# Kernel optimization log

Measured on AMD Instinct MI355X. Metric: run time of the kernel, lower is better.

## Reference

```python
import jax, jax.numpy as jnp
import numpy as np

CHUNK = 128  # single steady-state chunk tier (T divisible by 128)
DECAY_MIN = 0.005


def setup_inputs() -> dict:
    key = jax.random.key(0)
    k0, k1, k2, k3, k4 = jax.random.split(key, 5)
    B, H, T, K = 4, 16, 2048, 64
    r = jax.random.normal(k0, (B, H, T, K), jnp.float32) * 0.5
    k = jax.random.normal(k1, (B, H, T, K), jnp.float32) * 0.5
    v = jax.random.normal(k2, (B, H, T, K), jnp.float32)
    # log-space decay (negative); mild magnitude keeps exp() of cumulative
    # in-chunk decays within fp32 range (torch original upcasts to fp64)
    w = -(jax.random.uniform(k3, (B, H, T, K), jnp.float32) * 0.2 + 0.01)
    u = jax.random.normal(k4, (1, H, 1, K), jnp.float32) * 0.5
    wkv_state = jnp.zeros((B, H, K, K), jnp.float32)
    return {"r": r, "k": k, "v": v, "w": w, "u": u, "wkv_state": wkv_state}


def _chunked_wkv(r, k, v, w, u, wkv_state):
    B, H, T, K = r.shape
    Tc = CHUNK
    N = T // Tc
    # decay preprocessing (log space)
    w_decay = jnp.clip(jnp.exp(w), DECAY_MIN, None)
    w_log = jnp.log(w_decay)
    wc = w_log.reshape(B, H, N, Tc, K)
    wc_cum = jnp.cumsum(wc, axis=-2)                       # inclusive cumsum
    shifted = jnp.pad(wc_cum[..., :-1, :], ((0, 0), (0, 0), (0, 0), (1, 0), (0, 0)))
    ws = wc.sum(axis=-2, keepdims=True)                    # (B,H,N,1,K)
    w_inter = jnp.exp(ws - wc_cum)                          # (B,H,N,Tc,K)
    w_intra = jnp.exp(wc_cum - wc)
    ws_e = jnp.exp(jnp.swapaxes(ws, -1, -2))               # (B,H,N,K,1)

    rc = r.reshape(B, H, N, Tc, K)
    kc = k.reshape(B, H, N, Tc, K)
    vc = v.reshape(B, H, N, Tc, K)

    # numerically-centered intra-chunk decays (offset at chunk midpoint)
    off = shifted[..., Tc // 2:Tc // 2 + 1, :]
    r_dec = jnp.exp(shifted - off)
    k_inv = jnp.exp(off - wc_cum)

    # intra-chunk attention: strictly-lower-triangular + u-bonus diagonal
    a = jnp.einsum('bhnik,bhnjk->bhnij', rc * r_dec, kc * k_inv)
    a = jnp.tril(a, -1)
    diag = jnp.einsum('bhntk,bhntk->bhnt', rc, u[:, :, None] * kc)
    a = a + diag[..., :, None] * jnp.eye(Tc, dtype=a.dtype)
    out = jnp.einsum('bhnij,bhnjv->bhniv', a, vc)

    # inter-chunk: sequential state carry via scan
    wkv = jnp.einsum('bhntk,bhntv->bhnkv', kc * w_inter, vc)   # (B,H,N,K,K)

    def step(state, inp):
        ws_i, wkv_i = inp
        return state * ws_i + wkv_i, state

    ws_s = jnp.moveaxis(ws_e, 2, 0)    # (N,B,H,K,1)
    wkv_s = jnp.moveaxis(wkv, 2, 0)    # (N,B,H,K,K)
    final_state, states = jax.lax.scan(step, wkv_state, (ws_s, wkv_s))
    states = jnp.moveaxis(states, 0, 2)  # (B,H,N,K,K) — state entering chunk n

    out = out + jnp.einsum('bhntk,bhnkv->bhntv', rc * w_intra, states)
    return out.reshape(B, H, T, K), final_state


def reference(r, k, v, w, u, wkv_state):
    return _chunked_wkv(r, k, v, w, u, wkv_state)
```

## Files before the change

### kernel.cpp

```cpp
#include <hip/hip_runtime.h>

#define TC 128
#define KD 64
#define WLOG_MIN (-5.2983174f)

typedef __attribute__((ext_vector_type(8))) short short8;
typedef __attribute__((ext_vector_type(4))) short short4_t;
typedef __attribute__((ext_vector_type(4))) float f32x4;

__device__ __forceinline__ unsigned short f2bf(float x) {
  union { float f; unsigned int u; } c; c.f = x;
  unsigned int u = c.u + 0x7fffu + ((c.u >> 16) & 1u);
  return (unsigned short)(u >> 16);
}
__device__ __forceinline__ float bf2f(unsigned short x) {
  union { unsigned int u; float f; } c; c.u = ((unsigned int)x) << 16; return c.f;
}


__global__ __launch_bounds__(256, 3)
void rwkv_intra_mfma(const float* __restrict__ rr, const float* __restrict__ kk_,
                     const float* __restrict__ vv, const float* __restrict__ ww,
                     const float* __restrict__ uu, float* __restrict__ out,
                     unsigned short* __restrict__ wkv_u16, float* __restrict__ wse_ws,
                     unsigned short* __restrict__ rw_u16, unsigned short* __restrict__ diag_u16,
                     int H, int N) {
  __shared__ alignas(16) unsigned short rd_s[TC * KD];
  __shared__ alignas(16) unsigned short ki_s[TC * KD];
  __shared__ alignas(16) unsigned short vT_s[KD * TC];
  __shared__ alignas(16) unsigned char su_raw[5120];
  float* segtot = (float*)su_raw;
  unsigned short* Ast = (unsigned short*)su_raw;

  const int bid = blockIdx.x;
  const int n = bid % N, bh = bid / N, h = bh % H;
  const size_t base = ((size_t)bh * N + n) * (TC * KD);
  const float *rg = rr + base, *kg = kk_ + base, *vg = vv + base, *wg = ww + base;
  unsigned short* diagg = diag_u16 + (size_t)bid * TC;

  const int tid = threadIdx.x;
  const int lk = tid & 63;
  const int wv = tid >> 6;

  float wl[32];
  {
    float c = 0.f;
    #pragma unroll
    for (int tt = 0; tt < 32; ++tt) {
      wl[tt] = fmaxf(wg[(wv * 32 + tt) * KD + lk], WLOG_MIN);
      c += wl[tt];
    }
    segtot[wv * 64 + lk] = c;
  }
  __syncthreads();
  const float s0 = segtot[0 * 64 + lk], s1 = segtot[1 * 64 + lk];
  const float s2 = segtot[2 * 64 + lk], s3 = segtot[3 * 64 + lk];
  const float myoff = s0 + s1;
  const float segofs = (wv == 0) ? 0.f : (wv == 1) ? s0 : (wv == 2) ? (s0 + s1) : (s0 + s1 + s2);
  const float wsum = s0 + s1 + s2 + s3;
  const float wsoff_own = __expf(wsum - myoff);
  if (wv == 0) wse_ws[((size_t)bh * N + n) * KD + lk] = __expf(wsum);
  const float eoff = __expf(myoff);

  {
    float c = segofs;
    const float uk = uu[h * KD + lk];
    unsigned short* rwg = rw_u16 + base;
    short8 vb8;
    float darr[8];
    #pragma unroll
    for (int tt = 0; tt < 32; ++tt) {
      const int t = wv * 32 + tt;
      float rv = rg[t * KD + lk], kv = kg[t * KD + lk], vvv = vg[t * KD + lk];
      const int slot = (lk >> 3) ^ (t & 7) ^ ((t >> 3) & 7);
      const int nat = t * KD + (slot << 3) + (lk & 7);
      float e1 = __expf(c - myoff);
      rd_s[nat] = f2bf(rv * e1);
      rwg[t * KD + lk] = f2bf(rv * e1 * eoff);
      ki_s[nat] = f2bf(kv * __expf(myoff - c - wl[tt]));
      vb8[tt & 7] = (short)f2bf(vvv);
      darr[tt & 7] = rv * uk * kv;
      c += wl[tt];
      if ((tt & 7) == 7) {
        const int g = t >> 3;
        *(short8*)&vT_s[lk * TC + ((g ^ (lk & 7)) << 3)] = vb8;
        #pragma unroll
        for (int o = 32; o > 0; o >>= 1)
          #pragma unroll
          for (int q = 0; q < 8; ++q) darr[q] += __shfl_xor(darr[q], o, 64);
        if (lk == 0) {
          short8 dpk;
          #pragma unroll
          for (int q = 0; q < 8; ++q) dpk[q] = (short)f2bf(darr[q]);
          *(short8*)&diagg[g * 8] = dpk;
        }
      }
    }
  }
  __syncthreads();

  const int lane = tid & 63, quad = lane >> 4, l16 = lane & 15;

  {
    f32x4 acc[4] = {{0,0,0,0},{0,0,0,0},{0,0,0,0},{0,0,0,0}};
    const int kdg = wv * 2 + (l16 >> 3), kd7 = l16 & 7;
    #pragma unroll
    for (int ks = 0; ks < 4; ++ks) {
      short8 a;
      #pragma unroll
      for (int j = 0; j < 8; ++j) {
        const int t = ks * 32 + quad * 8 + j;
        a[j] = (short)ki_s[t * KD + (((kdg ^ (t & 7) ^ ((t >> 3) & 7)) << 3) + kd7)];
      }
      #pragma unroll
      for (int nn = 0; nn < 4; ++nn) {
        const int vd = nn * 16 + l16;
        short8 b = *(const short8*)&vT_s[vd * TC + (((ks * 4 + quad) ^ (vd & 7)) << 3)];
        acc[nn] = __builtin_amdgcn_mfma_f32_16x16x32_bf16(a, b, acc[nn], 0, 0, 0);
      }
    }
    float wso[4];
    #pragma unroll
    for (int reg = 0; reg < 4; ++reg) wso[reg] = __shfl(wsoff_own, wv * 16 + quad * 4 + reg, 64);
    unsigned short* wkvg = wkv_u16 + ((size_t)bh * N + n) * (KD * KD);
    #pragma unroll
    for (int nn = 0; nn < 4; ++nn)
      #pragma unroll
      for (int reg = 0; reg < 4; ++reg)
        wkvg[(wv * 16 + quad * 4 + reg) * KD + nn * 16 + l16] = f2bf(acc[nn][reg] * wso[reg]);
  }

  #pragma unroll
  for (int half = 0; half < 2; ++half) {
    const int ib = half ? (7 - wv) : wv;
    const int i0 = ib * 16;
    const int irow = i0 + l16;
    const int rsw = (irow & 7) ^ ((irow >> 3) & 7);
    short8 b0 = *(const short8*)&rd_s[irow * KD + ((quad ^ rsw) << 3)];
    short8 b1 = *(const short8*)&rd_s[irow * KD + (((4 + quad) ^ rsw) << 3)];
    const float diag_i = bf2f(diagg[irow]);
    f32x4 oacc[4] = {{0,0,0,0},{0,0,0,0},{0,0,0,0},{0,0,0,0}};
    const int npairs = (ib + 2) >> 1;
    unsigned short* astw = Ast + wv * 640;
    for (int jp = 0; jp < npairs; ++jp) {
      #pragma unroll
      for (int jj = 0; jj < 2; ++jj) {
        const int j = jp * 2 + jj;
        short4_t pk;
        if (j <= ib) {
          const int jrow = j * 16 + l16;
          const int jsw = (jrow & 7) ^ ((jrow >> 3) & 7);
          short8 a0 = *(const short8*)&ki_s[jrow * KD + ((quad ^ jsw) << 3)];
          short8 a1 = *(const short8*)&ki_s[jrow * KD + (((4 + quad) ^ jsw) << 3)];
          f32x4 at = {0, 0, 0, 0};
          at = __builtin_amdgcn_mfma_f32_16x16x32_bf16(a0, b0, at, 0, 0, 0);
          at = __builtin_amdgcn_mfma_f32_16x16x32_bf16(a1, b1, at, 0, 0, 0);
          #pragma unroll
          for (int reg = 0; reg < 4; ++reg) {
            const int je = j * 16 + quad * 4 + reg;
            float val = at[reg];
            if (j == ib) val = (je < irow) ? val : ((je == irow) ? diag_i : 0.f);
            pk[reg] = (short)f2bf(val);
          }
        } else {
          pk = (short4_t)0;
        }
        *(short4_t*)&astw[l16 * 40 + jj * 16 + quad * 4] = pk;
      }
      short8 af = *(const short8*)&astw[l16 * 40 + quad * 8];
      #pragma unroll
      for (int nn = 0; nn < 4; ++nn) {
        const int vd = nn * 16 + l16;
        short8 bv = *(const short8*)&vT_s[vd * TC + (((jp * 4 + quad) ^ (vd & 7)) << 3)];
        oacc[nn] = __builtin_amdgcn_mfma_f32_16x16x32_bf16(af, bv, oacc[nn], 0, 0, 0);
      }
    }
    float* og = out + base;
    #pragma unroll
    for (int nn = 0; nn < 4; ++nn)
      #pragma unroll
      for (int reg = 0; reg < 4; ++reg)
        og[(i0 + quad * 4 + reg) * KD + nn * 16 + l16] = oacc[nn][reg];
  }
}

__global__ __launch_bounds__(256)
void rwkv_scan_inter(const unsigned short* __restrict__ wkv_u16,
                     const float* __restrict__ wse_ws,
                     const float* __restrict__ st_in,
                     const unsigned short* __restrict__ rw_u16,
                     float* __restrict__ out, float* __restrict__ final_out, int N) {
  __shared__ alignas(16) unsigned short sT[16 * KD];
  const int bh = blockIdx.x >> 2, vq = blockIdx.x & 3;
  const int tid = threadIdx.x;
  const int vd_l = tid & 15;
  const int kd0 = (tid >> 4) * 4;
  const size_t sbase = (size_t)bh * (KD * KD);

  float stt[4];
  #pragma unroll
  for (int j = 0; j < 4; ++j) stt[j] = st_in[sbase + (kd0 + j) * KD + vq * 16 + vd_l];

  float nwk[4], nwe[4];
  #pragma unroll
  for (int j = 0; j < 4; ++j) {
    nwk[j] = bf2f(wkv_u16[(size_t)bh * N * (KD * KD) + (kd0 + j) * KD + vq * 16 + vd_l]);
    nwe[j] = wse_ws[(size_t)bh * N * KD + kd0 + j];
  }

  const int lane = tid & 63, wv = tid >> 6, quad = lane >> 4, l16 = lane & 15;
  for (int n = 0; n < N; ++n) {
    #pragma unroll
    for (int j = 0; j < 4; ++j) {
      const int kd = kd0 + j;
      sT[vd_l * KD + ((((kd >> 3) ^ (vd_l & 7)) << 3) | (kd & 7))] = f2bf(stt[j]);
    }
    __syncthreads();

    float cwk[4], cwe[4];
    #pragma unroll
    for (int j = 0; j < 4; ++j) { cwk[j] = nwk[j]; cwe[j] = nwe[j]; }
    if (n + 1 < N) {
      const size_t b2 = (size_t)bh * N + n + 1;
      #pragma unroll
      for (int j = 0; j < 4; ++j) {
        nwk[j] = bf2f(wkv_u16[b2 * (KD * KD) + (kd0 + j) * KD + vq * 16 + vd_l]);
        nwe[j] = wse_ws[b2 * KD + kd0 + j];
      }
    }

    const unsigned short* rwg = rw_u16 + ((size_t)bh * N + n) * (TC * KD);
    float* og = out + ((size_t)bh * N + n) * (TC * KD);
    #pragma unroll
    for (int half = 0; half < 2; ++half) {
      const int mt = wv + half * 4;
      const int trow = mt * 16 + l16;
      short8 a0 = *(const short8*)&rwg[trow * KD + quad * 8];
      short8 a1 = *(const short8*)&rwg[trow * KD + 32 + quad * 8];
      short8 b0 = *(const short8*)&sT[l16 * KD + ((quad ^ (l16 & 7)) << 3)];
      short8 b1 = *(const short8*)&sT[l16 * KD + (((4 + quad) ^ (l16 & 7)) << 3)];
      f32x4 acc = {0, 0, 0, 0};
      acc = __builtin_amdgcn_mfma_f32_16x16x32_bf16(a0, b0, acc, 0, 0, 0);
      acc = __builtin_amdgcn_mfma_f32_16x16x32_bf16(a1, b1, acc, 0, 0, 0);
      #pragma unroll
      for (int reg = 0; reg < 4; ++reg) {
        const size_t oi = (size_t)(mt * 16 + quad * 4 + reg) * KD + vq * 16 + l16;
        og[oi] += acc[reg];
      }
    }

    #pragma unroll
    for (int j = 0; j < 4; ++j) stt[j] = stt[j] * cwe[j] + cwk[j];
    __syncthreads();
  }
  #pragma unroll
  for (int j = 0; j < 4; ++j)
    final_out[sbase + (kd0 + j) * KD + vq * 16 + vd_l] = stt[j];
}

extern "C" void kernel_launch(void* const* d_in, const int* in_sizes, int n_in,
                              void* d_out, int out_size, void* d_ws, size_t ws_size,
                              hipStream_t stream) {
  const float* r = (const float*)d_in[0];
  const float* k = (const float*)d_in[1];
  const float* v = (const float*)d_in[2];
  const float* w = (const float*)d_in[3];
  const float* u = (const float*)d_in[4];
  const float* st0 = (const float*)d_in[5];
  float* out = (float*)d_out;

  const int BH = in_sizes[5] / (KD * KD);
  const int H = in_sizes[4] / KD;
  const int T = in_sizes[0] / (BH * KD);
  const int N = T / TC;

  unsigned short* wkv_u16 = (unsigned short*)d_ws;
  float* wse_ws = (float*)(wkv_u16 + (size_t)BH * N * KD * KD);
  unsigned short* rw_u16 = (unsigned short*)(wse_ws + (size_t)BH * N * KD);
  unsigned short* diag_u16 = rw_u16 + (size_t)BH * T * KD;
  float* final_out = out + (size_t)in_sizes[0];

  rwkv_intra_mfma<<<BH * N, 256, 0, stream>>>(r, k, v, w, u, out, wkv_u16, wse_ws,
                                              rw_u16, diag_u16, H, N);
  rwkv_scan_inter<<<BH * 4, 256, 0, stream>>>(wkv_u16, wse_ws, st0, rw_u16,
                                              out, final_out, N);
}
```

Before: 205.2 us.

## Replace sequential inter-chunk scan with per-chunk parallel state recompute; prefetch loads

The inter-chunk kernel no longer walks chunks sequentially with one block per (bh, quarter of v). It now launches one block per (bh, chunk), and each block recomputes its incoming state directly as a decayed sum over all earlier chunks' wkv contributions plus the initial state. This removes the serial N-step dependency and the per-step barriers, and raises the grid from BH*4 to BH*N blocks. The cost is redundant work that grows quadratically with N (about N/2 extra loads per block), plus a different rounding order from the running product of decays. Separately, the intra kernel double-buffers its r/k/v global loads in groups of 8 to overlap them with the exp and convert work.

```diff
diff --git a/kernel.cpp b/kernel.cpp
--- a/kernel.cpp
+++ b/kernel.cpp
@@ -52,6 +52,12 @@
     }
     segtot[wv * 64 + lk] = c;
   }
+  float rp[8], kp[8], vp[8];
+  #pragma unroll
+  for (int q = 0; q < 8; ++q) {
+    const int t = wv * 32 + q;
+    rp[q] = rg[t * KD + lk]; kp[q] = kg[t * KD + lk]; vp[q] = vg[t * KD + lk];
+  }
   __syncthreads();
   const float s0 = segtot[0 * 64 + lk], s1 = segtot[1 * 64 + lk];
   const float s2 = segtot[2 * 64 + lk], s3 = segtot[3 * 64 + lk];
@@ -66,34 +72,46 @@
     float c = segofs;
     const float uk = uu[h * KD + lk];
     unsigned short* rwg = rw_u16 + base;
-    short8 vb8;
-    float darr[8];
-    #pragma unroll
-    for (int tt = 0; tt < 32; ++tt) {
-      const int t = wv * 32 + tt;
-      float rv = rg[t * KD + lk], kv = kg[t * KD + lk], vvv = vg[t * KD + lk];
-      const int slot = (lk >> 3) ^ (t & 7) ^ ((t >> 3) & 7);
-      const int nat = t * KD + (slot << 3) + (lk & 7);
-      float e1 = __expf(c - myoff);
-      rd_s[nat] = f2bf(rv * e1);
-      rwg[t * KD + lk] = f2bf(rv * e1 * eoff);
-      ki_s[nat] = f2bf(kv * __expf(myoff - c - wl[tt]));
-      vb8[tt & 7] = (short)f2bf(vvv);
-      darr[tt & 7] = rv * uk * kv;
-      c += wl[tt];
-      if ((tt & 7) == 7) {
-        const int g = t >> 3;
-        *(short8*)&vT_s[lk * TC + ((g ^ (lk & 7)) << 3)] = vb8;
+    #pragma unroll
+    for (int g8 = 0; g8 < 4; ++g8) {
+      float rc8[8], kc8[8], vc8[8];
+      #pragma unroll
+      for (int q = 0; q < 8; ++q) { rc8[q] = rp[q]; kc8[q] = kp[q]; vc8[q] = vp[q]; }
+      if (g8 < 3) {
         #pragma unroll
-        for (int o = 32; o > 0; o >>= 1)
-          #pragma unroll
-          for (int q = 0; q < 8; ++q) darr[q] += __shfl_xor(darr[q], o, 64);
-        if (lk == 0) {
-          short8 dpk;
-          #pragma unroll
-          for (int q = 0; q < 8; ++q) dpk[q] = (short)f2bf(darr[q]);
-          *(short8*)&diagg[g * 8] = dpk;
+        for (int q = 0; q < 8; ++q) {
+          const int t = wv * 32 + (g8 + 1) * 8 + q;
+          rp[q] = rg[t * KD + lk]; kp[q] = kg[t * KD + lk]; vp[q] = vg[t * KD + lk];
         }
+      }
+      short8 vb8;
+      float darr[8];
+      #pragma unroll
+      for (int q = 0; q < 8; ++q) {
+        const int tt = g8 * 8 + q;
+        const int t = wv * 32 + tt;
+        float rv = rc8[q], kv = kc8[q], vvv = vc8[q];
+        const int slot = (lk >> 3) ^ (t & 7) ^ ((t >> 3) & 7);
+        const int nat = t * KD + (slot << 3) + (lk & 7);
+        float e1 = __expf(c - myoff);
+        rd_s[nat] = f2bf(rv * e1);
+        rwg[t * KD + lk] = f2bf(rv * e1 * eoff);
+        ki_s[nat] = f2bf(kv * __expf(myoff - c - wl[tt]));
+        vb8[q] = (short)f2bf(vvv);
+        darr[q] = rv * uk * kv;
+        c += wl[tt];
+      }
+      const int g = wv * 4 + g8;
+      *(short8*)&vT_s[lk * TC + ((g ^ (lk & 7)) << 3)] = vb8;
+      #pragma unroll
+      for (int o = 32; o > 0; o >>= 1)
+        #pragma unroll
+        for (int q = 0; q < 8; ++q) darr[q] += __shfl_xor(darr[q], o, 64);
+      if (lk == 0) {
+        short8 dpk;
+        #pragma unroll
+        for (int q = 0; q < 8; ++q) dpk[q] = (short)f2bf(darr[q]);
+        *(short8*)&diagg[g * 8] = dpk;
       }
     }
   }
@@ -185,77 +203,92 @@
 }
 
 __global__ __launch_bounds__(256)
-void rwkv_scan_inter(const unsigned short* __restrict__ wkv_u16,
-                     const float* __restrict__ wse_ws,
-                     const float* __restrict__ st_in,
-                     const unsigned short* __restrict__ rw_u16,
-                     float* __restrict__ out, float* __restrict__ final_out, int N) {
-  __shared__ alignas(16) unsigned short sT[16 * KD];
-  const int bh = blockIdx.x >> 2, vq = blockIdx.x & 3;
+void rwkv_state_inter(const unsigned short* __restrict__ wkv_u16,
+                      const float* __restrict__ wse_ws,
+                      const float* __restrict__ st_in,
+                      const unsigned short* __restrict__ rw_u16,
+                      float* __restrict__ out, float* __restrict__ final_out, int N) {
+  __shared__ alignas(16) unsigned short sT[KD * KD];
+  const int bid = blockIdx.x;
+  const int n = bid % N, bh = bid / N;
   const int tid = threadIdx.x;
-  const int vd_l = tid & 15;
-  const int kd0 = (tid >> 4) * 4;
-  const size_t sbase = (size_t)bh * (KD * KD);
-
-  float stt[4];
-  #pragma unroll
-  for (int j = 0; j < 4; ++j) stt[j] = st_in[sbase + (kd0 + j) * KD + vq * 16 + vd_l];
-
-  float nwk[4], nwe[4];
-  #pragma unroll
-  for (int j = 0; j < 4; ++j) {
-    nwk[j] = bf2f(wkv_u16[(size_t)bh * N * (KD * KD) + (kd0 + j) * KD + vq * 16 + vd_l]);
-    nwe[j] = wse_ws[(size_t)bh * N * KD + kd0 + j];
-  }
-
-  const int lane = tid & 63, wv = tid >> 6, quad = lane >> 4, l16 = lane & 15;
-  for (int n = 0; n < N; ++n) {
-    #pragma unroll
-    for (int j = 0; j < 4; ++j) {
-      const int kd = kd0 + j;
-      sT[vd_l * KD + ((((kd >> 3) ^ (vd_l & 7)) << 3) | (kd & 7))] = f2bf(stt[j]);
-    }
-    __syncthreads();
-
-    float cwk[4], cwe[4];
-    #pragma unroll
-    for (int j = 0; j < 4; ++j) { cwk[j] = nwk[j]; cwe[j] = nwe[j]; }
-    if (n + 1 < N) {
-      const size_t b2 = (size_t)bh * N + n + 1;
-      #pragma unroll
-      for (int j = 0; j < 4; ++j) {
-        nwk[j] = bf2f(wkv_u16[b2 * (KD * KD) + (kd0 + j) * KD + vq * 16 + vd_l]);
-        nwe[j] = wse_ws[b2 * KD + kd0 + j];
-      }
-    }
-
-    const unsigned short* rwg = rw_u16 + ((size_t)bh * N + n) * (TC * KD);
-    float* og = out + ((size_t)bh * N + n) * (TC * KD);
-    #pragma unroll
-    for (int half = 0; half < 2; ++half) {
-      const int mt = wv + half * 4;
-      const int trow = mt * 16 + l16;
-      short8 a0 = *(const short8*)&rwg[trow * KD + quad * 8];
-      short8 a1 = *(const short8*)&rwg[trow * KD + 32 + quad * 8];
-      short8 b0 = *(const short8*)&sT[l16 * KD + ((quad ^ (l16 & 7)) << 3)];
-      short8 b1 = *(const short8*)&sT[l16 * KD + (((4 + quad) ^ (l16 & 7)) << 3)];
-      f32x4 acc = {0, 0, 0, 0};
-      acc = __builtin_amdgcn_mfma_f32_16x16x32_bf16(a0, b0, acc, 0, 0, 0);
-      acc = __builtin_amdgcn_mfma_f32_16x16x32_bf16(a1, b1, acc, 0, 0, 0);
-      #pragma unroll
-      for (int reg = 0; reg < 4; ++reg) {
-        const size_t oi = (size_t)(mt * 16 + quad * 4 + reg) * KD + vq * 16 + l16;
-        og[oi] += acc[reg];
-      }
-    }
-
-    #pragma unroll
-    for (int j = 0; j < 4; ++j) stt[j] = stt[j] * cwe[j] + cwk[j];
-    __syncthreads();
-  }
-  #pragma unroll
-  for (int j = 0; j < 4; ++j)
-    final_out[sbase + (kd0 + j) * KD + vq * 16 + vd_l] = stt[j];
+  const int kd1 = tid >> 3;
+  const int kd2 = kd1 + 32;
+  const int v0 = (tid & 7) * 8;
+  const size_t cbase = (size_t)bh * N;
+
+  float S1[8], S2[8];
+  float P1 = 1.f, P2 = 1.f;
+  #pragma unroll
+  for (int j = 0; j < 8; ++j) { S1[j] = 0.f; S2[j] = 0.f; }
+  for (int m = n - 1; m >= 0; --m) {
+    const unsigned short* wk = wkv_u16 + (cbase + m) * (KD * KD);
+    short8 a1 = *(const short8*)&wk[kd1 * KD + v0];
+    short8 a2 = *(const short8*)&wk[kd2 * KD + v0];
+    float e1 = wse_ws[(cbase + m) * KD + kd1];
+    float e2 = wse_ws[(cbase + m) * KD + kd2];
+    #pragma unroll
+    for (int j = 0; j < 8; ++j) {
+      S1[j] += P1 * bf2f((unsigned short)a1[j]);
+      S2[j] += P2 * bf2f((unsigned short)a2[j]);
+    }
+    P1 *= e1; P2 *= e2;
+  }
+  {
+    const float* s0g = st_in + (size_t)bh * (KD * KD);
+    #pragma unroll
+    for (int j = 0; j < 8; ++j) {
+      S1[j] += P1 * s0g[kd1 * KD + v0 + j];
+      S2[j] += P2 * s0g[kd2 * KD + v0 + j];
+    }
+  }
+  if (n == N - 1) {
+    const unsigned short* wk = wkv_u16 + (cbase + N - 1) * (KD * KD);
+    short8 a1 = *(const short8*)&wk[kd1 * KD + v0];
+    short8 a2 = *(const short8*)&wk[kd2 * KD + v0];
+    float e1 = wse_ws[(cbase + N - 1) * KD + kd1];
+    float e2 = wse_ws[(cbase + N - 1) * KD + kd2];
+    float* fo = final_out + (size_t)bh * (KD * KD);
+    #pragma unroll
+    for (int j = 0; j < 8; ++j) {
+      fo[kd1 * KD + v0 + j] = S1[j] * e1 + bf2f((unsigned short)a1[j]);
+      fo[kd2 * KD + v0 + j] = S2[j] * e2 + bf2f((unsigned short)a2[j]);
+    }
+  }
+  #pragma unroll
+  for (int j = 0; j < 8; ++j) {
+    const int vd = v0 + j;
+    const int rs = (vd & 7) ^ ((vd >> 3) & 7);
+    sT[vd * KD + ((((kd1 >> 3) ^ rs) << 3) | (kd1 & 7))] = f2bf(S1[j]);
+    sT[vd * KD + ((((kd2 >> 3) ^ rs) << 3) | (kd2 & 7))] = f2bf(S2[j]);
+  }
+  __syncthreads();
+
+  const int lane = tid & 63, wvv = tid >> 6, quad = lane >> 4, l16 = lane & 15;
+  const unsigned short* rwg = rw_u16 + (cbase + n) * (TC * KD);
+  float* og = out + (cbase + n) * (TC * KD);
+  #pragma unroll
+  for (int half = 0; half < 2; ++half) {
+    const int mt = wvv + half * 4;
+    const int trow = mt * 16 + l16;
+    short8 a0 = *(const short8*)&rwg[trow * KD + quad * 8];
+    short8 a1 = *(const short8*)&rwg[trow * KD + 32 + quad * 8];
+    f32x4 acc[4] = {{0,0,0,0},{0,0,0,0},{0,0,0,0},{0,0,0,0}};
+    #pragma unroll
+    for (int nn = 0; nn < 4; ++nn) {
+      const int vd = nn * 16 + l16;
+      const int rs = (vd & 7) ^ ((vd >> 3) & 7);
+      short8 b0 = *(const short8*)&sT[vd * KD + ((quad ^ rs) << 3)];
+      short8 b1 = *(const short8*)&sT[vd * KD + (((4 + quad) ^ rs) << 3)];
+      acc[nn] = __builtin_amdgcn_mfma_f32_16x16x32_bf16(a0, b0, acc[nn], 0, 0, 0);
+      acc[nn] = __builtin_amdgcn_mfma_f32_16x16x32_bf16(a1, b1, acc[nn], 0, 0, 0);
+    }
+    #pragma unroll
+    for (int nn = 0; nn < 4; ++nn)
+      #pragma unroll
+      for (int reg = 0; reg < 4; ++reg)
+        og[(size_t)(mt * 16 + quad * 4 + reg) * KD + nn * 16 + l16] += acc[nn][reg];
+  }
 }
 
 extern "C" void kernel_launch(void* const* d_in, const int* in_sizes, int n_in,
@@ -282,6 +315,6 @@
 
   rwkv_intra_mfma<<<BH * N, 256, 0, stream>>>(r, k, v, w, u, out, wkv_u16, wse_ws,
                                               rw_u16, diag_u16, H, N);
-  rwkv_scan_inter<<<BH * 4, 256, 0, stream>>>(wkv_u16, wse_ws, st0, rw_u16,
-                                              out, final_out, N);
-}
+  rwkv_state_inter<<<BH * N, 256, 0, stream>>>(wkv_u16, wse_ws, st0, rw_u16,
+                                               out, final_out, N);
+}
```

Result: no change. 206.9 us (+0.8%).

## Parallelize inter-chunk state over chunks and vectorize intra preprocessing loads

Applied to the files above, without the earlier changes.

The sequential scan kernel, which used BH*4 blocks each looping over all N chunks, is replaced by BH*N*2 independent blocks. Each block rebuilds its incoming state by summing the earlier chunks' wkv contributions weighted by their decay products, then applies it with MFMA. This removes the serial dependency and low occupancy of the scan at the cost of redundant work that grows with the number of preceding chunks. The intra kernel's preprocessing now uses float4 loads, with each lane owning 4 channels and 8 timesteps, and computes the segment prefix through shuffles, cutting scalar global loads.

```diff
diff --git a/kernel.cpp b/kernel.cpp
--- a/kernel.cpp
+++ b/kernel.cpp
@@ -39,67 +39,118 @@
   unsigned short* diagg = diag_u16 + (size_t)bid * TC;
 
   const int tid = threadIdx.x;
-  const int lk = tid & 63;
   const int wv = tid >> 6;
-
-  float wl[32];
-  {
-    float c = 0.f;
-    #pragma unroll
-    for (int tt = 0; tt < 32; ++tt) {
-      wl[tt] = fmaxf(wg[(wv * 32 + tt) * KD + lk], WLOG_MIN);
-      c += wl[tt];
-    }
-    segtot[wv * 64 + lk] = c;
+  const int lane = tid & 63;
+  const int tq = lane >> 4;
+  const int c16 = lane & 15;
+  const int kd0 = c16 * 4;
+
+  float4 wl4[8];
+  float4 pre;
+  {
+    float4 loc = make_float4(0.f, 0.f, 0.f, 0.f);
+    #pragma unroll
+    for (int i = 0; i < 8; ++i) {
+      const int t = wv * 32 + tq * 8 + i;
+      float4 w4 = *(const float4*)&wg[t * KD + kd0];
+      wl4[i] = make_float4(fmaxf(w4.x, WLOG_MIN), fmaxf(w4.y, WLOG_MIN),
+                           fmaxf(w4.z, WLOG_MIN), fmaxf(w4.w, WLOG_MIN));
+      loc.x += wl4[i].x; loc.y += wl4[i].y; loc.z += wl4[i].z; loc.w += wl4[i].w;
+    }
+    float4 p0, p1, p2;
+    p0.x = __shfl(loc.x, c16, 64);      p0.y = __shfl(loc.y, c16, 64);
+    p0.z = __shfl(loc.z, c16, 64);      p0.w = __shfl(loc.w, c16, 64);
+    p1.x = __shfl(loc.x, 16 + c16, 64); p1.y = __shfl(loc.y, 16 + c16, 64);
+    p1.z = __shfl(loc.z, 16 + c16, 64); p1.w = __shfl(loc.w, 16 + c16, 64);
+    p2.x = __shfl(loc.x, 32 + c16, 64); p2.y = __shfl(loc.y, 32 + c16, 64);
+    p2.z = __shfl(loc.z, 32 + c16, 64); p2.w = __shfl(loc.w, 32 + c16, 64);
+    pre = make_float4(0.f, 0.f, 0.f, 0.f);
+    if (tq >= 1) { pre.x += p0.x; pre.y += p0.y; pre.z += p0.z; pre.w += p0.w; }
+    if (tq >= 2) { pre.x += p1.x; pre.y += p1.y; pre.z += p1.z; pre.w += p1.w; }
+    if (tq >= 3) { pre.x += p2.x; pre.y += p2.y; pre.z += p2.z; pre.w += p2.w; }
+    if (tq == 3) {
+      float4 st4 = make_float4(pre.x + loc.x, pre.y + loc.y, pre.z + loc.z, pre.w + loc.w);
+      *(float4*)&segtot[wv * 64 + kd0] = st4;
+    }
   }
   __syncthreads();
-  const float s0 = segtot[0 * 64 + lk], s1 = segtot[1 * 64 + lk];
-  const float s2 = segtot[2 * 64 + lk], s3 = segtot[3 * 64 + lk];
-  const float myoff = s0 + s1;
-  const float segofs = (wv == 0) ? 0.f : (wv == 1) ? s0 : (wv == 2) ? (s0 + s1) : (s0 + s1 + s2);
-  const float wsum = s0 + s1 + s2 + s3;
-  const float wsoff_own = __expf(wsum - myoff);
-  if (wv == 0) wse_ws[((size_t)bh * N + n) * KD + lk] = __expf(wsum);
-  const float eoff = __expf(myoff);
-
-  {
-    float c = segofs;
-    const float uk = uu[h * KD + lk];
+
+  float wsoff_own;
+  {
+    const float t0 = segtot[0 * 64 + lane], t1 = segtot[1 * 64 + lane];
+    const float t2 = segtot[2 * 64 + lane], t3 = segtot[3 * 64 + lane];
+    wsoff_own = __expf(t2 + t3);
+    if (wv == 0) wse_ws[((size_t)bh * N + n) * KD + lane] = __expf(t0 + t1 + t2 + t3);
+  }
+  float4 s0 = *(const float4*)&segtot[0 * 64 + kd0];
+  float4 s1 = *(const float4*)&segtot[1 * 64 + kd0];
+  float4 myoff4 = make_float4(s0.x + s1.x, s0.y + s1.y, s0.z + s1.z, s0.w + s1.w);
+  float4 segofs4;
+  {
+    float4 s2 = *(const float4*)&segtot[2 * 64 + kd0];
+    segofs4 = make_float4(0.f, 0.f, 0.f, 0.f);
+    if (wv >= 1) { segofs4.x += s0.x; segofs4.y += s0.y; segofs4.z += s0.z; segofs4.w += s0.w; }
+    if (wv >= 2) { segofs4.x += s1.x; segofs4.y += s1.y; segofs4.z += s1.z; segofs4.w += s1.w; }
+    if (wv >= 3) { segofs4.x += s2.x; segofs4.y += s2.y; segofs4.z += s2.z; segofs4.w += s2.w; }
+  }
+  const float4 eoff4 = make_float4(__expf(myoff4.x), __expf(myoff4.y),
+                                   __expf(myoff4.z), __expf(myoff4.w));
+
+  {
+    float4 c4 = make_float4(segofs4.x + pre.x, segofs4.y + pre.y,
+                            segofs4.z + pre.z, segofs4.w + pre.w);
+    const float4 uk4 = *(const float4*)&uu[h * KD + kd0];
     unsigned short* rwg = rw_u16 + base;
-    short8 vb8;
-    float darr[8];
-    #pragma unroll
-    for (int tt = 0; tt < 32; ++tt) {
-      const int t = wv * 32 + tt;
-      float rv = rg[t * KD + lk], kv = kg[t * KD + lk], vvv = vg[t * KD + lk];
-      const int slot = (lk >> 3) ^ (t & 7) ^ ((t >> 3) & 7);
-      const int nat = t * KD + (slot << 3) + (lk & 7);
-      float e1 = __expf(c - myoff);
-      rd_s[nat] = f2bf(rv * e1);
-      rwg[t * KD + lk] = f2bf(rv * e1 * eoff);
-      ki_s[nat] = f2bf(kv * __expf(myoff - c - wl[tt]));
-      vb8[tt & 7] = (short)f2bf(vvv);
-      darr[tt & 7] = rv * uk * kv;
-      c += wl[tt];
-      if ((tt & 7) == 7) {
-        const int g = t >> 3;
-        *(short8*)&vT_s[lk * TC + ((g ^ (lk & 7)) << 3)] = vb8;
-        #pragma unroll
-        for (int o = 32; o > 0; o >>= 1)
-          #pragma unroll
-          for (int q = 0; q < 8; ++q) darr[q] += __shfl_xor(darr[q], o, 64);
-        if (lk == 0) {
-          short8 dpk;
-          #pragma unroll
-          for (int q = 0; q < 8; ++q) dpk[q] = (short)f2bf(darr[q]);
-          *(short8*)&diagg[g * 8] = dpk;
-        }
-      }
+    short8 vb8[4];
+    float dpart[8];
+    const int g = wv * 4 + tq;
+    #pragma unroll
+    for (int i = 0; i < 8; ++i) {
+      const int t = wv * 32 + tq * 8 + i;
+      float4 r4 = *(const float4*)&rg[t * KD + kd0];
+      float4 k4 = *(const float4*)&kg[t * KD + kd0];
+      float4 v4 = *(const float4*)&vg[t * KD + kd0];
+      float4 e1 = make_float4(__expf(c4.x - myoff4.x), __expf(c4.y - myoff4.y),
+                              __expf(c4.z - myoff4.z), __expf(c4.w - myoff4.w));
+      const int slot = (c16 >> 1) ^ (i) ^ (g & 7);
+      const int nat = t * KD + (slot << 3) + ((c16 & 1) << 2);
+      short4_t rdp, rwp, kip;
+      rdp[0] = (short)f2bf(r4.x * e1.x); rdp[1] = (short)f2bf(r4.y * e1.y);
+      rdp[2] = (short)f2bf(r4.z * e1.z); rdp[3] = (short)f2bf(r4.w * e1.w);
+      rwp[0] = (short)f2bf(r4.x * e1.x * eoff4.x); rwp[1] = (short)f2bf(r4.y * e1.y * eoff4.y);
+      rwp[2] = (short)f2bf(r4.z * e1.z * eoff4.z); rwp[3] = (short)f2bf(r4.w * e1.w * eoff4.w);
+      kip[0] = (short)f2bf(k4.x * __expf(myoff4.x - c4.x - wl4[i].x));
+      kip[1] = (short)f2bf(k4.y * __expf(myoff4.y - c4.y - wl4[i].y));
+      kip[2] = (short)f2bf(k4.z * __expf(myoff4.z - c4.z - wl4[i].z));
+      kip[3] = (short)f2bf(k4.w * __expf(myoff4.w - c4.w - wl4[i].w));
+      *(short4_t*)&rd_s[nat] = rdp;
+      *(short4_t*)&ki_s[nat] = kip;
+      *(short4_t*)&rwg[t * KD + kd0] = rwp;
+      vb8[0][i] = (short)f2bf(v4.x); vb8[1][i] = (short)f2bf(v4.y);
+      vb8[2][i] = (short)f2bf(v4.z); vb8[3][i] = (short)f2bf(v4.w);
+      dpart[i] = r4.x * uk4.x * k4.x + r4.y * uk4.y * k4.y +
+                 r4.z * uk4.z * k4.z + r4.w * uk4.w * k4.w;
+      c4.x += wl4[i].x; c4.y += wl4[i].y; c4.z += wl4[i].z; c4.w += wl4[i].w;
+    }
+    #pragma unroll
+    for (int j = 0; j < 4; ++j) {
+      const int vd = kd0 + j;
+      *(short8*)&vT_s[vd * TC + ((g ^ (vd & 7)) << 3)] = vb8[j];
+    }
+    #pragma unroll
+    for (int o = 1; o < 16; o <<= 1)
+      #pragma unroll
+      for (int i = 0; i < 8; ++i) dpart[i] += __shfl_xor(dpart[i], o, 64);
+    if (c16 == 0) {
+      short8 dpk;
+      #pragma unroll
+      for (int i = 0; i < 8; ++i) dpk[i] = (short)f2bf(dpart[i]);
+      *(short8*)&diagg[g * 8] = dpk;
     }
   }
   __syncthreads();
 
-  const int lane = tid & 63, quad = lane >> 4, l16 = lane & 15;
+  const int quad = lane >> 4, l16 = lane & 15;
 
   {
     f32x4 acc[4] = {{0,0,0,0},{0,0,0,0},{0,0,0,0},{0,0,0,0}};
@@ -185,77 +236,101 @@
 }
 
 __global__ __launch_bounds__(256)
-void rwkv_scan_inter(const unsigned short* __restrict__ wkv_u16,
-                     const float* __restrict__ wse_ws,
-                     const float* __restrict__ st_in,
-                     const unsigned short* __restrict__ rw_u16,
-                     float* __restrict__ out, float* __restrict__ final_out, int N) {
-  __shared__ alignas(16) unsigned short sT[16 * KD];
-  const int bh = blockIdx.x >> 2, vq = blockIdx.x & 3;
+void rwkv_state_inter(const unsigned short* __restrict__ wkv_u16,
+                      const float* __restrict__ wse_ws,
+                      const float* __restrict__ st_in,
+                      const unsigned short* __restrict__ rw_u16,
+                      float* __restrict__ out, float* __restrict__ final_out, int N) {
+  __shared__ alignas(16) unsigned short sT[32 * KD];
+  const int bid = blockIdx.x;
+  const int half = bid & 1;
+  const int cn = bid >> 1;
+  const int n = cn % N, bh = cn / N;
   const int tid = threadIdx.x;
-  const int vd_l = tid & 15;
-  const int kd0 = (tid >> 4) * 4;
-  const size_t sbase = (size_t)bh * (KD * KD);
-
-  float stt[4];
-  #pragma unroll
-  for (int j = 0; j < 4; ++j) stt[j] = st_in[sbase + (kd0 + j) * KD + vq * 16 + vd_l];
-
-  float nwk[4], nwe[4];
-  #pragma unroll
-  for (int j = 0; j < 4; ++j) {
-    nwk[j] = bf2f(wkv_u16[(size_t)bh * N * (KD * KD) + (kd0 + j) * KD + vq * 16 + vd_l]);
-    nwe[j] = wse_ws[(size_t)bh * N * KD + kd0 + j];
-  }
-
-  const int lane = tid & 63, wv = tid >> 6, quad = lane >> 4, l16 = lane & 15;
-  for (int n = 0; n < N; ++n) {
-    #pragma unroll
-    for (int j = 0; j < 4; ++j) {
-      const int kd = kd0 + j;
-      sT[vd_l * KD + ((((kd >> 3) ^ (vd_l & 7)) << 3) | (kd & 7))] = f2bf(stt[j]);
-    }
-    __syncthreads();
-
-    float cwk[4], cwe[4];
-    #pragma unroll
-    for (int j = 0; j < 4; ++j) { cwk[j] = nwk[j]; cwe[j] = nwe[j]; }
-    if (n + 1 < N) {
-      const size_t b2 = (size_t)bh * N + n + 1;
-      #pragma unroll
-      for (int j = 0; j < 4; ++j) {
-        nwk[j] = bf2f(wkv_u16[b2 * (KD * KD) + (kd0 + j) * KD + vq * 16 + vd_l]);
-        nwe[j] = wse_ws[b2 * KD + kd0 + j];
-      }
-    }
-
-    const unsigned short* rwg = rw_u16 + ((size_t)bh * N + n) * (TC * KD);
-    float* og = out + ((size_t)bh * N + n) * (TC * KD);
-    #pragma unroll
-    for (int half = 0; half < 2; ++half) {
-      const int mt = wv + half * 4;
-      const int trow = mt * 16 + l16;
-      short8 a0 = *(const short8*)&rwg[trow * KD + quad * 8];
-      short8 a1 = *(const short8*)&rwg[trow * KD + 32 + quad * 8];
-      short8 b0 = *(const short8*)&sT[l16 * KD + ((quad ^ (l16 & 7)) << 3)];
-      short8 b1 = *(const short8*)&sT[l16 * KD + (((4 + quad) ^ (l16 & 7)) << 3)];
-      f32x4 acc = {0, 0, 0, 0};
-      acc = __builtin_amdgcn_mfma_f32_16x16x32_bf16(a0, b0, acc, 0, 0, 0);
-      acc = __builtin_amdgcn_mfma_f32_16x16x32_bf16(a1, b1, acc, 0, 0, 0);
-      #pragma unroll
-      for (int reg = 0; reg < 4; ++reg) {
-        const size_t oi = (size_t)(mt * 16 + quad * 4 + reg) * KD + vq * 16 + l16;
-        og[oi] += acc[reg];
-      }
-    }
-
-    #pragma unroll
-    for (int j = 0; j < 4; ++j) stt[j] = stt[j] * cwe[j] + cwk[j];
-    __syncthreads();
-  }
-  #pragma unroll
-  for (int j = 0; j < 4; ++j)
-    final_out[sbase + (kd0 + j) * KD + vq * 16 + vd_l] = stt[j];
+  const size_t cbase = (size_t)bh * N;
+
+  const int lane = tid & 63, wvv = tid >> 6, quad = lane >> 4, l16 = lane & 15;
+
+  const unsigned short* rwg = rw_u16 + (cbase + n) * (TC * KD);
+  short8 afr[4];
+  #pragma unroll
+  for (int half2 = 0; half2 < 2; ++half2) {
+    const int trow = (wvv + half2 * 4) * 16 + l16;
+    afr[half2 * 2 + 0] = *(const short8*)&rwg[trow * KD + quad * 8];
+    afr[half2 * 2 + 1] = *(const short8*)&rwg[trow * KD + 32 + quad * 8];
+  }
+
+  const int kd = tid >> 2;
+  const int vv = (tid & 3) * 8 + half * 32;
+  float S[8];
+  #pragma unroll
+  for (int j = 0; j < 8; ++j) S[j] = 0.f;
+  float P = 1.f;
+  {
+    int m = n - 1;
+    short8 a_nx = {0,0,0,0,0,0,0,0};
+    float e_nx = 0.f;
+    if (m >= 0) {
+      a_nx = *(const short8*)&wkv_u16[(cbase + m) * (KD * KD) + kd * KD + vv];
+      e_nx = wse_ws[(cbase + m) * KD + kd];
+    }
+    while (m >= 0) {
+      short8 a = a_nx; float e = e_nx;
+      if (m - 1 >= 0) {
+        a_nx = *(const short8*)&wkv_u16[(cbase + m - 1) * (KD * KD) + kd * KD + vv];
+        e_nx = wse_ws[(cbase + m - 1) * KD + kd];
+      }
+      #pragma unroll
+      for (int j = 0; j < 8; ++j) S[j] += P * bf2f((unsigned short)a[j]);
+      P *= e;
+      --m;
+    }
+  }
+  {
+    const float* s0g = st_in + (size_t)bh * (KD * KD) + kd * KD + vv;
+    float4 q0 = *(const float4*)&s0g[0];
+    float4 q1 = *(const float4*)&s0g[4];
+    S[0] += P * q0.x; S[1] += P * q0.y; S[2] += P * q0.z; S[3] += P * q0.w;
+    S[4] += P * q1.x; S[5] += P * q1.y; S[6] += P * q1.z; S[7] += P * q1.w;
+  }
+  if (n == N - 1) {
+    const unsigned short* wk = wkv_u16 + (cbase + N - 1) * (KD * KD) + kd * KD + vv;
+    short8 a = *(const short8*)wk;
+    const float e = wse_ws[(cbase + N - 1) * KD + kd];
+    float* fo = final_out + (size_t)bh * (KD * KD) + kd * KD + vv;
+    #pragma unroll
+    for (int j = 0; j < 8; ++j) fo[j] = S[j] * e + bf2f((unsigned short)a[j]);
+  }
+  #pragma unroll
+  for (int j = 0; j < 8; ++j) {
+    const int vd_l = (tid & 3) * 8 + j;
+    const int rs = (vd_l & 7) ^ ((vd_l >> 3) & 7);
+    sT[vd_l * KD + ((((kd >> 3) ^ rs) << 3) | (kd & 7))] = f2bf(S[j]);
+  }
+  __syncthreads();
+
+  float* og = out + (cbase + n) * (TC * KD);
+  #pragma unroll
+  for (int half2 = 0; half2 < 2; ++half2) {
+    const int mt = wvv + half2 * 4;
+    short8 a0 = afr[half2 * 2 + 0];
+    short8 a1 = afr[half2 * 2 + 1];
+    f32x4 acc[2] = {{0,0,0,0},{0,0,0,0}};
+    #pragma unroll
+    for (int nn = 0; nn < 2; ++nn) {
+      const int vd_l = nn * 16 + l16;
+      const int rs = (vd_l & 7) ^ ((vd_l >> 3) & 7);
+      short8 b0 = *(const short8*)&sT[vd_l * KD + ((quad ^ rs) << 3)];
+      short8 b1 = *(const short8*)&sT[vd_l * KD + (((4 + quad) ^ rs) << 3)];
+      acc[nn] = __builtin_amdgcn_mfma_f32_16x16x32_bf16(a0, b0, acc[nn], 0, 0, 0);
+      acc[nn] = __builtin_amdgcn_mfma_f32_16x16x32_bf16(a1, b1, acc[nn], 0, 0, 0);
+    }
+    #pragma unroll
+    for (int nn = 0; nn < 2; ++nn)
+      #pragma unroll
+      for (int reg = 0; reg < 4; ++reg)
+        og[(size_t)(mt * 16 + quad * 4 + reg) * KD + half * 32 + nn * 16 + l16] += acc[nn][reg];
+  }
 }
 
 extern "C" void kernel_launch(void* const* d_in, const int* in_sizes, int n_in,
@@ -282,6 +357,6 @@
 
   rwkv_intra_mfma<<<BH * N, 256, 0, stream>>>(r, k, v, w, u, out, wkv_u16, wse_ws,
                                               rw_u16, diag_u16, H, N);
-  rwkv_scan_inter<<<BH * 4, 256, 0, stream>>>(wkv_u16, wse_ws, st0, rw_u16,
-                                              out, final_out, N);
-}
+  rwkv_state_inter<<<BH * N * 2, 256, 0, stream>>>(wkv_u16, wse_ws, st0, rw_u16,
+                                                   out, final_out, N);
+}
```

New measurement: 214.9 us. 1.05x slower.
